# Kernel optimization log

Measured on AMD Instinct MI355X. Metric: run time of the kernel, lower is better.

Reference implementation:

```python
import jax, jax.numpy as jnp
import numpy as np

B, T, TEMP, H, M = 2048, 168, 128, 1024, 48


def lstm_cell(x, h, c, Wih, Whh, bih, bhh):
    # PyTorch gate order: i, f, g, o
    gates = x @ Wih.T + h @ Whh.T + bih + bhh  # [B, 4H]
    i, f, g, o = jnp.split(gates, 4, axis=-1)
    i = jax.nn.sigmoid(i)
    f = jax.nn.sigmoid(f)
    g = jnp.tanh(g)
    o = jax.nn.sigmoid(o)
    c_new = f * c + i * g
    h_new = o * jnp.tanh(c_new)
    return h_new, c_new


def setup_inputs() -> dict:
    key = jax.random.key(0)
    ks = jax.random.split(key, 12)
    s_e = 1.0 / np.sqrt(H)
    u = lambda k, shape: jax.random.uniform(k, shape, jnp.float32, -s_e, s_e)
    return {
        "temp_seq": jax.random.normal(ks[0], (B, T, TEMP), jnp.float32),
        "avg_speeds": jax.random.normal(ks[1], (B, M), jnp.float32),
        "enc_Wih": u(ks[2], (4 * H, TEMP)),
        "enc_Whh": u(ks[3], (4 * H, H)),
        "enc_bih": u(ks[4], (4 * H,)),
        "enc_bhh": u(ks[5], (4 * H,)),
        "dec_Wih": u(ks[6], (4 * H, TEMP + 1)),
        "dec_Whh": u(ks[7], (4 * H, H)),
        "dec_bih": u(ks[8], (4 * H,)),
        "dec_bhh": u(ks[9], (4 * H,)),
        "fc_W": u(ks[10], (TEMP, H)),
        "fc_b": u(ks[11], (TEMP,)),
    }


def reference(temp_seq, avg_speeds, enc_Wih, enc_Whh, enc_bih, enc_bhh,
              dec_Wih, dec_Whh, dec_bih, dec_bhh, fc_W, fc_b):
    b = temp_seq.shape[0]
    h0 = jnp.zeros((b, H), temp_seq.dtype)
    c0 = jnp.zeros((b, H), temp_seq.dtype)

    # Encoder: LSTM over time, keep only final (h, c)
    def enc_step(carry, x_t):
        h, c = carry
        h, c = lstm_cell(x_t, h, c, enc_Wih, enc_Whh, enc_bih, enc_bhh)
        return (h, c), None

    (h_n, c_n), _ = jax.lax.scan(enc_step, (h0, c0), jnp.swapaxes(temp_seq, 0, 1))

    input_temp0 = temp_seq[:, -1, :]  # [B, TEMP]

    def dec_step(carry, speed_t):
        h, c, x_temp = carry
        x = jnp.concatenate([x_temp, speed_t[:, None]], axis=-1)  # [B, TEMP+1]
        h, c = lstm_cell(x, h, c, dec_Wih, dec_Whh, dec_bih, dec_bhh)
        pred = h @ fc_W.T + fc_b  # [B, TEMP]
        return (h, c, pred), pred

    _, preds = jax.lax.scan(dec_step, (h_n, c_n, input_temp0),
                            jnp.swapaxes(avg_speeds, 0, 1))
    return jnp.swapaxes(preds, 0, 1)  # [B, M, TEMP]
```

## Files before the change

### kernel.cpp

```cpp
#include <hip/hip_runtime.h>
#include <stdint.h>

#define B_SZ   2048
#define T_ENC  168
#define TEMPD  128
#define HID    1024
#define M_DEC  48

typedef _Float16 f16;
typedef _Float16 half8 __attribute__((ext_vector_type(8)));
typedef float    f32x4 __attribute__((ext_vector_type(4)));

__device__ __forceinline__ float sigf(float x)   { return 1.0f / (1.0f + __expf(-x)); }
__device__ __forceinline__ float tanhf_(float x) { return 2.0f / (1.0f + __expf(-2.0f * x)) - 1.0f; }

__device__ __forceinline__ void gld16(const void* g, void* l) {
    __builtin_amdgcn_global_load_lds(
        (const __attribute__((address_space(1))) void*)g,
        (__attribute__((address_space(3))) void*)l, 16, 0, 0);
}

#define WAITV6() asm volatile("s_waitcnt vmcnt(6)" ::: "memory")
#define WAITV0() asm volatile("s_waitcnt vmcnt(0)" ::: "memory")
#define SBAR()   do { __builtin_amdgcn_sched_barrier(0); \
                      __builtin_amdgcn_s_barrier();      \
                      __builtin_amdgcn_sched_barrier(0); } while (0)

__global__ void prep_xseq(const float* __restrict__ temp_seq, f16* __restrict__ xseq)
{
    size_t i4 = ((size_t)blockIdx.x * blockDim.x + threadIdx.x) * 4;
    size_t b  = i4 / (T_ENC * TEMPD);
    size_t r  = i4 - b * (T_ENC * TEMPD);
    size_t t  = r >> 7;
    size_t d  = r & 127;
    float4 v = *(const float4*)(temp_seq + i4);
    f16* o = xseq + ((t * B_SZ) + b) * TEMPD + d;
    o[0] = (f16)v.x; o[1] = (f16)v.y; o[2] = (f16)v.z; o[3] = (f16)v.w;
}

__global__ void prep_misc(
    const float* __restrict__ encWih, const float* __restrict__ encWhh,
    const float* __restrict__ decWih, const float* __restrict__ decWhh,
    const float* __restrict__ encbih, const float* __restrict__ encbhh,
    const float* __restrict__ decbih, const float* __restrict__ decbhh,
    const float* __restrict__ fcW,
    f16* __restrict__ Wenc, f16* __restrict__ Wdec0, f16* __restrict__ fcWh,
    float* __restrict__ enc_b, float* __restrict__ dec_b, float* __restrict__ wlast)
{
    const int NW = 4 * HID * (TEMPD + HID);
    for (int idx = blockIdx.x * blockDim.x + threadIdx.x; idx < NW;
         idx += gridDim.x * blockDim.x) {
        int j = idx / (TEMPD + HID);
        int k = idx - j * (TEMPD + HID);
        Wenc[idx]  = (f16)(k < TEMPD ? encWih[j * TEMPD + k]
                                     : encWhh[(size_t)j * HID + (k - TEMPD)]);
        Wdec0[idx] = (f16)(k < TEMPD ? decWih[j * (TEMPD + 1) + k]
                                     : decWhh[(size_t)j * HID + (k - TEMPD)]);
        if (idx < TEMPD * HID) fcWh[idx] = (f16)fcW[idx];
        if (idx < 4 * HID) {
            enc_b[idx] = encbih[idx] + encbhh[idx];
            dec_b[idx] = decbih[idx] + decbhh[idx];
            wlast[idx] = decWih[idx * (TEMPD + 1) + TEMPD];
        }
    }
}

__global__ __launch_bounds__(256)
void prep_fold(
    const float* __restrict__ decWih, const float* __restrict__ decWhh,
    const float* __restrict__ decbih, const float* __restrict__ decbhh,
    const float* __restrict__ fcW,    const float* __restrict__ fcb,
    f16* __restrict__ WdecF, float* __restrict__ biasF)
{
    __shared__ float wih[16][TEMPD];
    __shared__ float fcbL[TEMPD];
    const int tid = threadIdx.x;
    const int j0  = blockIdx.x * 16;
    for (int i = tid; i < 16 * TEMPD; i += 256) {
        int r = i >> 7, p = i & 127;
        wih[r][p] = decWih[(size_t)(j0 + r) * (TEMPD + 1) + p];
    }
    if (tid < TEMPD) fcbL[tid] = fcb[tid];
    __syncthreads();
    for (int kk = 0; kk < 4; ++kk) {
        int k = kk * 256 + tid;
        float acc[16];
        #pragma unroll
        for (int r = 0; r < 16; ++r) acc[r] = decWhh[(size_t)(j0 + r) * HID + k];
        for (int p = 0; p < TEMPD; ++p) {
            float w = fcW[(size_t)p * HID + k];
            #pragma unroll
            for (int r = 0; r < 16; ++r) acc[r] += wih[r][p] * w;
        }
        #pragma unroll
        for (int r = 0; r < 16; ++r) WdecF[(size_t)(j0 + r) * HID + k] = (f16)acc[r];
    }
    if (tid < 16) {
        float b = decbih[j0 + tid] + decbhh[j0 + tid];
        for (int p = 0; p < TEMPD; ++p) b += wih[tid][p] * fcbL[p];
        biasF[j0 + tid] = b;
    }
}

template <int FULLK, int DEC>
__global__ __launch_bounds__(512, 2)
void lstm_step(
    const f16* __restrict__ xsrc,
    const f16* __restrict__ h_in, f16* __restrict__ h_out, float* __restrict__ c,
    const f16* __restrict__ W,
    const float* __restrict__ bias,
    const float* __restrict__ wlast, const float* __restrict__ speeds, int m_step)
{
    constexpr int NKC = FULLK ? 18 : 16;
    constexpr int WS  = FULLK ? (HID + TEMPD) : HID;

    __shared__ half8 ldsA[3][1024];
    __shared__ half8 ldsW[3][2048];

    const int tid  = threadIdx.x;
    const int id   = blockIdx.x;
    const int swzb = (id & 7) * 32 + (id >> 3);
    const int bm   = swzb & 15;
    const int bn   = swzb >> 4;
    const int lane = tid & 63;
    const int wid  = tid >> 6;
    const int wr   = wid >> 2;
    const int wc   = wid & 3;

    f32x4 acc[4][4];
    #pragma unroll
    for (int g = 0; g < 4; ++g)
        #pragma unroll
        for (int mr = 0; mr < 4; ++mr)
            acc[g][mr] = (f32x4){0.f, 0.f, 0.f, 0.f};

    auto stageA = [&](int b, int kc) {
        if (FULLK && kc < 2) {
            #pragma unroll
            for (int it = 0; it < 2; ++it) {
                int p = wid * 128 + it * 64 + lane;
                int row = p >> 3, s = p & 7;
                gld16(xsrc + (size_t)(bm * 128 + row) * TEMPD + kc * 64 + ((s ^ (row & 7)) << 3),
                      &ldsA[b][wid * 128 + it * 64]);
            }
        } else {
            const int k0 = kc * 64 - (FULLK ? TEMPD : 0);
            #pragma unroll
            for (int it = 0; it < 2; ++it) {
                int p = wid * 128 + it * 64 + lane;
                int row = p >> 3, s = p & 7;
                gld16(h_in + (size_t)(bm * 128 + row) * HID + k0 + ((s ^ (row & 7)) << 3),
                      &ldsA[b][wid * 128 + it * 64]);
            }
        }
    };
    auto stageW = [&](int b, int kc) {
        const int k0 = kc * 64;
        #pragma unroll
        for (int it = 0; it < 4; ++it) {
            int p = wid * 256 + it * 64 + lane;
            int r = p >> 3, s = p & 7;
            int g = r >> 6, j = r & 63;
            gld16(W + (size_t)(g * HID + bn * 64 + j) * WS + k0 + ((s ^ (r & 7)) << 3),
                  &ldsW[b][wid * 256 + it * 64]);
        }
    };

    stageA(0, 0); stageW(0, 0);
    stageA(1, 1); stageW(1, 1);

    int cur = 0;
    for (int kc = 0; kc < NKC; ++kc) {
        if (kc == NKC - 1) { WAITV0(); } else { WAITV6(); }
        SBAR();
        if (kc + 2 < NKC) {
            int nb = cur + 2; if (nb >= 3) nb -= 3;
            stageA(nb, kc + 2);
            stageW(nb, kc + 2);
        }
        #pragma unroll
        for (int s = 0; s < 2; ++s) {
            const int ks = s * 4 + (lane >> 4);
            half8 af[4];
            #pragma unroll
            for (int mr = 0; mr < 4; ++mr) {
                int row = wr * 64 + mr * 16 + (lane & 15);
                af[mr] = ldsA[cur][row * 8 + (ks ^ (row & 7))];
            }
            half8 bf[4];
            #pragma unroll
            for (int g = 0; g < 4; ++g) {
                int r = g * 64 + wc * 16 + (lane & 15);
                bf[g] = ldsW[cur][r * 8 + (ks ^ (r & 7))];
            }
            __builtin_amdgcn_s_setprio(1);
            #pragma unroll
            for (int g = 0; g < 4; ++g)
                #pragma unroll
                for (int mr = 0; mr < 4; ++mr)
                    acc[g][mr] = __builtin_amdgcn_mfma_f32_16x16x32_f16(af[mr], bf[g], acc[g][mr], 0, 0, 0);
            __builtin_amdgcn_s_setprio(0);
        }
        cur = (cur == 2) ? 0 : cur + 1;
    }

    const int col_g = bn * 64 + wc * 16 + (lane & 15);
    const float bi  = bias[col_g];
    const float bf_ = bias[HID + col_g];
    const float bg  = bias[2 * HID + col_g];
    const float bo  = bias[3 * HID + col_g];
    float wli = 0.f, wlf = 0.f, wlg = 0.f, wlo = 0.f;
    if (DEC) {
        wli = wlast[col_g];
        wlf = wlast[HID + col_g];
        wlg = wlast[2 * HID + col_g];
        wlo = wlast[3 * HID + col_g];
    }
    #pragma unroll
    for (int mr = 0; mr < 4; ++mr) {
        #pragma unroll
        for (int q = 0; q < 4; ++q) {
            int row_g = bm * 128 + wr * 64 + mr * 16 + (lane >> 4) * 4 + q;
            float pi = acc[0][mr][q] + bi;
            float pf = acc[1][mr][q] + bf_;
            float pg = acc[2][mr][q] + bg;
            float po = acc[3][mr][q] + bo;
            if (DEC) {
                float sp = speeds[(size_t)row_g * M_DEC + m_step];
                pi += sp * wli; pf += sp * wlf; pg += sp * wlg; po += sp * wlo;
            }
            float ii = sigf(pi), ff = sigf(pf), gg = tanhf_(pg), oo = sigf(po);
            size_t idx = (size_t)row_g * HID + col_g;
            float cn = ff * c[idx] + ii * gg;
            c[idx] = cn;
            h_out[idx] = (f16)(oo * tanhf_(cn));
        }
    }
}

__global__ __launch_bounds__(256, 2)
void fc_batch(const f16* __restrict__ hist, const f16* __restrict__ fcWh,
              const float* __restrict__ fcb, float* __restrict__ out, int mbase)
{
    __shared__ half8 ldsA[32 * 8];
    __shared__ half8 ldsW[128 * 8];
    const int tid  = threadIdx.x;
    const int lane = tid & 63;
    const int wid  = tid >> 6;
    const int wr   = wid >> 1;
    const int wc   = wid & 1;
    const int bm   = blockIdx.x;
    const int slot = bm >> 6;
    const int b0   = (bm & 63) * 32;
    const f16* hrow = hist + (size_t)slot * (B_SZ * HID) + (size_t)b0 * HID;
    const int  mm   = mbase + slot;

    f32x4 acc[4];
    #pragma unroll
    for (int nr = 0; nr < 4; ++nr) acc[nr] = (f32x4){0.f, 0.f, 0.f, 0.f};

    for (int kc = 0; kc < HID / 64; ++kc) {
        const int k0 = kc * 64;
        {
            int row = tid >> 3, s = tid & 7;
            gld16(hrow + (size_t)row * HID + k0 + ((s ^ (row & 7)) << 3), &ldsA[wid * 64]);
        }
        #pragma unroll
        for (int it = 0; it < 4; ++it) {
            int p = wid * 256 + it * 64 + lane;
            int row = p >> 3, s = p & 7;
            gld16(fcWh + (size_t)row * HID + k0 + ((s ^ (row & 7)) << 3), &ldsW[wid * 256 + it * 64]);
        }
        __syncthreads();
        #pragma unroll
        for (int s2 = 0; s2 < 2; ++s2) {
            int arow = wr * 16 + (lane & 15);
            int slotk = s2 * 4 + (lane >> 4);
            half8 a = ldsA[arow * 8 + (slotk ^ (arow & 7))];
            #pragma unroll
            for (int nr = 0; nr < 4; ++nr) {
                int brow = wc * 64 + nr * 16 + (lane & 15);
                half8 bfr = ldsW[brow * 8 + (slotk ^ (brow & 7))];
                acc[nr] = __builtin_amdgcn_mfma_f32_16x16x32_f16(a, bfr, acc[nr], 0, 0, 0);
            }
        }
        __syncthreads();
    }
    #pragma unroll
    for (int nr = 0; nr < 4; ++nr)
        #pragma unroll
        for (int q = 0; q < 4; ++q) {
            int rloc = wr * 16 + (lane >> 4) * 4 + q;
            int col  = wc * 64 + nr * 16 + (lane & 15);
            out[(size_t)(b0 + rloc) * (M_DEC * TEMPD) + (size_t)mm * TEMPD + col] = acc[nr][q] + fcb[col];
        }
}

extern "C" void kernel_launch(void* const* d_in, const int* in_sizes, int n_in,
                              void* d_out, int out_size, void* d_ws, size_t ws_size,
                              hipStream_t stream)
{
    (void)in_sizes; (void)n_in; (void)out_size; (void)ws_size;
    const float* temp_seq   = (const float*)d_in[0];
    const float* avg_speeds = (const float*)d_in[1];
    const float* enc_Wih    = (const float*)d_in[2];
    const float* enc_Whh    = (const float*)d_in[3];
    const float* enc_bih    = (const float*)d_in[4];
    const float* enc_bhh    = (const float*)d_in[5];
    const float* dec_Wih    = (const float*)d_in[6];
    const float* dec_Whh    = (const float*)d_in[7];
    const float* dec_bih    = (const float*)d_in[8];
    const float* dec_bhh    = (const float*)d_in[9];
    const float* fc_W       = (const float*)d_in[10];
    const float* fc_b       = (const float*)d_in[11];
    float* out = (float*)d_out;

    char* ws = (char*)d_ws;
    size_t off = 0;
    auto alloc = [&](size_t bytes) -> void* {
        void* p = ws + off;
        off += (bytes + 255) & ~(size_t)255;
        return p;
    };
    const size_t SLOT = (size_t)B_SZ * HID;
    f16*   Wenc   = (f16*)alloc((size_t)4 * HID * (TEMPD + HID) * 2);
    f16*   Wdec0  = (f16*)alloc((size_t)4 * HID * (TEMPD + HID) * 2);
    f16*   WdecF  = (f16*)alloc((size_t)4 * HID * HID * 2);
    f16*   fcWh   = (f16*)alloc((size_t)TEMPD * HID * 2);
    float* enc_b  = (float*)alloc((size_t)4 * HID * 4);
    float* dec_b  = (float*)alloc((size_t)4 * HID * 4);
    float* biasF  = (float*)alloc((size_t)4 * HID * 4);
    float* wlast  = (float*)alloc((size_t)4 * HID * 4);
    f16*   hA     = (f16*)alloc(SLOT * 2);
    f16*   hB     = (f16*)alloc(SLOT * 2);
    float* cbuf   = (float*)alloc(SLOT * 4);
    f16*   xseq   = (f16*)alloc((size_t)T_ENC * B_SZ * TEMPD * 2);
    f16*   hist   = (f16*)alloc(16 * SLOT * 2);

    hipMemsetAsync(hA,   0, SLOT * 2, stream);
    hipMemsetAsync(cbuf, 0, SLOT * 4, stream);

    prep_xseq<<<(B_SZ * T_ENC * TEMPD / 4 + 255) / 256, 256, 0, stream>>>(temp_seq, xseq);
    prep_misc<<<8192, 256, 0, stream>>>(
        enc_Wih, enc_Whh, dec_Wih, dec_Whh,
        enc_bih, enc_bhh, dec_bih, dec_bhh, fc_W,
        Wenc, Wdec0, fcWh, enc_b, dec_b, wlast);
    prep_fold<<<256, 256, 0, stream>>>(
        dec_Wih, dec_Whh, dec_bih, dec_bhh, fc_W, fc_b, WdecF, biasF);

    f16* hbuf[2] = {hA, hB};
    for (int t = 0; t < T_ENC; ++t) {
        lstm_step<1, 0><<<256, 512, 0, stream>>>(
            xseq + (size_t)t * (B_SZ * TEMPD),
            hbuf[t & 1], hbuf[(t + 1) & 1], cbuf,
            Wenc, enc_b, nullptr, nullptr, 0);
    }
    for (int m = 0; m < M_DEC; ++m) {
        const f16* hin = (m == 0) ? hA : hist + ((size_t)((m - 1) & 15)) * SLOT;
        f16* hout = hist + ((size_t)(m & 15)) * SLOT;
        if (m == 0) {
            lstm_step<1, 1><<<256, 512, 0, stream>>>(
                xseq + (size_t)(T_ENC - 1) * (B_SZ * TEMPD),
                hin, hout, cbuf, Wdec0, dec_b, wlast, avg_speeds, 0);
        } else {
            lstm_step<0, 1><<<256, 512, 0, stream>>>(
                nullptr, hin, hout, cbuf, WdecF, biasF, wlast, avg_speeds, m);
        }
        if ((m & 15) == 15) {
            fc_batch<<<1024, 256, 0, stream>>>(hist, fcWh, fc_b, out, m - 15);
        }
    }
}
```

Baseline: 6.821 ms.

## Interleave split weight staging with fragment reads and MFMA, prefetch cell state

The LSTM gate GEMM main loop is restructured. Each K-chunk now reads LDS fragments and issues MFMAs in two halves, and the next chunk's weight staging is split across those halves, with explicit lgkmcnt waits and barriers between them. The c state and decoder speed values are loaded into registers before the loop, so the epilogue no longer waits on those global loads. The goal is better overlap of global-to-LDS traffic with MFMA work. In exchange it adds four barriers per chunk instead of one, and 32 more live registers under a two-blocks-per-CU launch bound.

```diff
diff --git a/kernel.cpp b/kernel.cpp
--- a/kernel.cpp
+++ b/kernel.cpp
@@ -25,6 +25,9 @@
 #define SBAR()   do { __builtin_amdgcn_sched_barrier(0); \
                       __builtin_amdgcn_s_barrier();      \
                       __builtin_amdgcn_sched_barrier(0); } while (0)
+#define LGKM0()  do { asm volatile("s_waitcnt lgkmcnt(0)" ::: "memory"); \
+                      __builtin_amdgcn_sched_barrier(0); } while (0)
+#define MEMFENCE() asm volatile("" ::: "memory")
 
 __global__ void prep_xseq(const float* __restrict__ temp_seq, f16* __restrict__ xseq)
 {
@@ -154,10 +157,11 @@
             }
         }
     };
-    auto stageW = [&](int b, int kc) {
+    auto stageWhalf = [&](int b, int kc, int half) {
         const int k0 = kc * 64;
         #pragma unroll
-        for (int it = 0; it < 4; ++it) {
+        for (int it2 = 0; it2 < 2; ++it2) {
+            int it = half * 2 + it2;
             int p = wid * 256 + it * 64 + lane;
             int r = p >> 3, s = p & 7;
             int g = r >> 6, j = r & 63;
@@ -166,43 +170,32 @@
         }
     };
 
-    stageA(0, 0); stageW(0, 0);
-    stageA(1, 1); stageW(1, 1);
-
-    int cur = 0;
-    for (int kc = 0; kc < NKC; ++kc) {
-        if (kc == NKC - 1) { WAITV0(); } else { WAITV6(); }
-        SBAR();
-        if (kc + 2 < NKC) {
-            int nb = cur + 2; if (nb >= 3) nb -= 3;
-            stageA(nb, kc + 2);
-            stageW(nb, kc + 2);
-        }
-        #pragma unroll
-        for (int s = 0; s < 2; ++s) {
-            const int ks = s * 4 + (lane >> 4);
-            half8 af[4];
+    half8 af[4], bf[4];
+    auto rdfrags = [&](int cb, int s) {
+        const int ks = s * 4 + (lane >> 4);
+        #pragma unroll
+        for (int mr = 0; mr < 4; ++mr) {
+            int row = wr * 64 + mr * 16 + (lane & 15);
+            af[mr] = ldsA[cb][row * 8 + (ks ^ (row & 7))];
+        }
+        #pragma unroll
+        for (int g = 0; g < 4; ++g) {
+            int r = g * 64 + wc * 16 + (lane & 15);
+            bf[g] = ldsW[cb][r * 8 + (ks ^ (r & 7))];
+        }
+    };
+    auto mfma16 = [&]() {
+        __builtin_amdgcn_s_setprio(1);
+        #pragma unroll
+        for (int g = 0; g < 4; ++g)
             #pragma unroll
-            for (int mr = 0; mr < 4; ++mr) {
-                int row = wr * 64 + mr * 16 + (lane & 15);
-                af[mr] = ldsA[cur][row * 8 + (ks ^ (row & 7))];
-            }
-            half8 bf[4];
-            #pragma unroll
-            for (int g = 0; g < 4; ++g) {
-                int r = g * 64 + wc * 16 + (lane & 15);
-                bf[g] = ldsW[cur][r * 8 + (ks ^ (r & 7))];
-            }
-            __builtin_amdgcn_s_setprio(1);
-            #pragma unroll
-            for (int g = 0; g < 4; ++g)
-                #pragma unroll
-                for (int mr = 0; mr < 4; ++mr)
-                    acc[g][mr] = __builtin_amdgcn_mfma_f32_16x16x32_f16(af[mr], bf[g], acc[g][mr], 0, 0, 0);
-            __builtin_amdgcn_s_setprio(0);
-        }
-        cur = (cur == 2) ? 0 : cur + 1;
-    }
+            for (int mr = 0; mr < 4; ++mr)
+                acc[g][mr] = __builtin_amdgcn_mfma_f32_16x16x32_f16(af[mr], bf[g], acc[g][mr], 0, 0, 0);
+        __builtin_amdgcn_s_setprio(0);
+    };
+
+    stageA(0, 0); stageWhalf(0, 0, 0); stageWhalf(0, 0, 1);
+    MEMFENCE();
 
     const int col_g = bn * 64 + wc * 16 + (lane & 15);
     const float bi  = bias[col_g];
@@ -210,12 +203,53 @@
     const float bg  = bias[2 * HID + col_g];
     const float bo  = bias[3 * HID + col_g];
     float wli = 0.f, wlf = 0.f, wlg = 0.f, wlo = 0.f;
+    float sp_r[4];
     if (DEC) {
         wli = wlast[col_g];
         wlf = wlast[HID + col_g];
         wlg = wlast[2 * HID + col_g];
         wlo = wlast[3 * HID + col_g];
-    }
+        #pragma unroll
+        for (int mr = 0; mr < 4; ++mr) {
+            int row_g = bm * 128 + wr * 64 + mr * 16 + (lane >> 4) * 4;
+            sp_r[mr] = 0.f;
+            (void)row_g;
+        }
+    }
+    float creg[4][4];
+    float spq[4][4];
+    #pragma unroll
+    for (int mr = 0; mr < 4; ++mr)
+        #pragma unroll
+        for (int q = 0; q < 4; ++q) {
+            int row_g = bm * 128 + wr * 64 + mr * 16 + (lane >> 4) * 4 + q;
+            creg[mr][q] = c[(size_t)row_g * HID + col_g];
+            if (DEC) spq[mr][q] = speeds[(size_t)row_g * M_DEC + m_step];
+        }
+
+    stageA(1, 1); stageWhalf(1, 1, 0); stageWhalf(1, 1, 1);
+    WAITV6();
+    SBAR();
+
+    int cur = 0;
+    for (int kc = 0; kc < NKC; ++kc) {
+        int nb = cur + 2; if (nb >= 3) nb -= 3;
+        rdfrags(cur, 0);
+        if (kc + 2 < NKC) { stageA(nb, kc + 2); stageWhalf(nb, kc + 2, 0); }
+        SBAR();
+        LGKM0();
+        mfma16();
+        SBAR();
+        rdfrags(cur, 1);
+        if (kc + 2 < NKC) { stageWhalf(nb, kc + 2, 1); WAITV6(); }
+        else              { WAITV0(); }
+        SBAR();
+        LGKM0();
+        mfma16();
+        SBAR();
+        cur = (cur == 2) ? 0 : cur + 1;
+    }
+
     #pragma unroll
     for (int mr = 0; mr < 4; ++mr) {
         #pragma unroll
@@ -226,12 +260,12 @@
             float pg = acc[2][mr][q] + bg;
             float po = acc[3][mr][q] + bo;
             if (DEC) {
-                float sp = speeds[(size_t)row_g * M_DEC + m_step];
+                float sp = spq[mr][q];
                 pi += sp * wli; pf += sp * wlf; pg += sp * wlg; po += sp * wlo;
             }
             float ii = sigf(pi), ff = sigf(pf), gg = tanhf_(pg), oo = sigf(po);
             size_t idx = (size_t)row_g * HID + col_g;
-            float cn = ff * c[idx] + ii * gg;
+            float cn = ff * creg[mr][q] + ii * gg;
             c[idx] = cn;
             h_out[idx] = (f16)(oo * tanhf_(cn));
         }
```

New measurement: 6.273 ms. 8.0% less time.

## Load pre-tiled LSTM weights directly into registers and drop LDS weight staging

Applied to the files above, without the earlier changes.

Adds a prep kernel that rearranges the gate weight matrices into MFMA-fragment order, so each wave can read its B operands straight from global memory into registers instead of staging them through LDS. The step kernel moves to 256-thread blocks covering 32 hidden columns, with 512 blocks per step, and switches from a three-stage pipeline with explicit vmcnt waits to two LDS buffers for the activations only, synchronised with __syncthreads. This cuts LDS traffic and footprint, which may allow more resident blocks. In exchange, each weight element is fetched by more blocks and register pressure goes up because two fragment sets are held in flight.

```diff
diff --git a/kernel.cpp b/kernel.cpp
--- a/kernel.cpp
+++ b/kernel.cpp
@@ -19,12 +19,6 @@
         (const __attribute__((address_space(1))) void*)g,
         (__attribute__((address_space(3))) void*)l, 16, 0, 0);
 }
-
-#define WAITV6() asm volatile("s_waitcnt vmcnt(6)" ::: "memory")
-#define WAITV0() asm volatile("s_waitcnt vmcnt(0)" ::: "memory")
-#define SBAR()   do { __builtin_amdgcn_sched_barrier(0); \
-                      __builtin_amdgcn_s_barrier();      \
-                      __builtin_amdgcn_sched_barrier(0); } while (0)
 
 __global__ void prep_xseq(const float* __restrict__ temp_seq, f16* __restrict__ xseq)
 {
@@ -102,30 +96,48 @@
     }
 }
 
+__global__ void prep_tileW(const f16* __restrict__ Wsrc, f16* __restrict__ Wt,
+                           int NKC, int WS)
+{
+    int idx = blockIdx.x * blockDim.x + threadIdx.x;
+    int total = 32 * NKC * 16 * 64;
+    if (idx >= total) return;
+    int lane = idx & 63;
+    int f    = idx >> 6;
+    int wc   = f & 1;
+    int g    = (f >> 1) & 3;
+    int s    = (f >> 3) & 1;
+    int kc   = (f >> 4) % NKC;
+    int bn   = (f >> 4) / NKC;
+    int row  = g * HID + bn * 32 + wc * 16 + (lane & 15);
+    int k0   = kc * 64 + s * 32 + (lane >> 4) * 8;
+    *(half8*)(Wt + (size_t)idx * 8) = *(const half8*)(Wsrc + (size_t)row * WS + k0);
+}
+
 template <int FULLK, int DEC>
-__global__ __launch_bounds__(512, 2)
+__global__ __launch_bounds__(256, 2)
 void lstm_step(
     const f16* __restrict__ xsrc,
     const f16* __restrict__ h_in, f16* __restrict__ h_out, float* __restrict__ c,
-    const f16* __restrict__ W,
+    const f16* __restrict__ Wt,
     const float* __restrict__ bias,
     const float* __restrict__ wlast, const float* __restrict__ speeds, int m_step)
 {
     constexpr int NKC = FULLK ? 18 : 16;
-    constexpr int WS  = FULLK ? (HID + TEMPD) : HID;
-
-    __shared__ half8 ldsA[3][1024];
-    __shared__ half8 ldsW[3][2048];
+
+    __shared__ half8 ldsA[2][1024];
 
     const int tid  = threadIdx.x;
-    const int id   = blockIdx.x;
-    const int swzb = (id & 7) * 32 + (id >> 3);
-    const int bm   = swzb & 15;
-    const int bn   = swzb >> 4;
     const int lane = tid & 63;
     const int wid  = tid >> 6;
-    const int wr   = wid >> 2;
-    const int wc   = wid & 3;
+    const int wr   = wid >> 1;
+    const int wc   = wid & 1;
+    const int id   = blockIdx.x;
+    const int swzb = (id & 7) * 64 + (id >> 3);
+    const int bn   = swzb >> 4;
+    const int bm   = swzb & 15;
+
+    const half8* wtb = (const half8*)Wt + ((size_t)bn * NKC * 16) * 64 + wc * 64 + lane;
 
     f32x4 acc[4][4];
     #pragma unroll
@@ -137,47 +149,29 @@
     auto stageA = [&](int b, int kc) {
         if (FULLK && kc < 2) {
             #pragma unroll
-            for (int it = 0; it < 2; ++it) {
-                int p = wid * 128 + it * 64 + lane;
+            for (int it = 0; it < 4; ++it) {
+                int p = wid * 256 + it * 64 + lane;
                 int row = p >> 3, s = p & 7;
                 gld16(xsrc + (size_t)(bm * 128 + row) * TEMPD + kc * 64 + ((s ^ (row & 7)) << 3),
-                      &ldsA[b][wid * 128 + it * 64]);
+                      &ldsA[b][wid * 256 + it * 64]);
             }
         } else {
             const int k0 = kc * 64 - (FULLK ? TEMPD : 0);
             #pragma unroll
-            for (int it = 0; it < 2; ++it) {
-                int p = wid * 128 + it * 64 + lane;
+            for (int it = 0; it < 4; ++it) {
+                int p = wid * 256 + it * 64 + lane;
                 int row = p >> 3, s = p & 7;
                 gld16(h_in + (size_t)(bm * 128 + row) * HID + k0 + ((s ^ (row & 7)) << 3),
-                      &ldsA[b][wid * 128 + it * 64]);
+                      &ldsA[b][wid * 256 + it * 64]);
             }
         }
     };
-    auto stageW = [&](int b, int kc) {
-        const int k0 = kc * 64;
-        #pragma unroll
-        for (int it = 0; it < 4; ++it) {
-            int p = wid * 256 + it * 64 + lane;
-            int r = p >> 3, s = p & 7;
-            int g = r >> 6, j = r & 63;
-            gld16(W + (size_t)(g * HID + bn * 64 + j) * WS + k0 + ((s ^ (r & 7)) << 3),
-                  &ldsW[b][wid * 256 + it * 64]);
-        }
+    auto loadW = [&](half8 (&wf)[8], int kc) {
+        const half8* p = wtb + (size_t)kc * (16 * 64);
+        #pragma unroll
+        for (int f = 0; f < 8; ++f) wf[f] = p[f * 128];
     };
-
-    stageA(0, 0); stageW(0, 0);
-    stageA(1, 1); stageW(1, 1);
-
-    int cur = 0;
-    for (int kc = 0; kc < NKC; ++kc) {
-        if (kc == NKC - 1) { WAITV0(); } else { WAITV6(); }
-        SBAR();
-        if (kc + 2 < NKC) {
-            int nb = cur + 2; if (nb >= 3) nb -= 3;
-            stageA(nb, kc + 2);
-            stageW(nb, kc + 2);
-        }
+    auto compute = [&](int b, const half8 (&wf)[8]) {
         #pragma unroll
         for (int s = 0; s < 2; ++s) {
             const int ks = s * 4 + (lane >> 4);
@@ -185,26 +179,32 @@
             #pragma unroll
             for (int mr = 0; mr < 4; ++mr) {
                 int row = wr * 64 + mr * 16 + (lane & 15);
-                af[mr] = ldsA[cur][row * 8 + (ks ^ (row & 7))];
-            }
-            half8 bf[4];
-            #pragma unroll
-            for (int g = 0; g < 4; ++g) {
-                int r = g * 64 + wc * 16 + (lane & 15);
-                bf[g] = ldsW[cur][r * 8 + (ks ^ (r & 7))];
+                af[mr] = ldsA[b][row * 8 + (ks ^ (row & 7))];
             }
             __builtin_amdgcn_s_setprio(1);
             #pragma unroll
             for (int g = 0; g < 4; ++g)
                 #pragma unroll
                 for (int mr = 0; mr < 4; ++mr)
-                    acc[g][mr] = __builtin_amdgcn_mfma_f32_16x16x32_f16(af[mr], bf[g], acc[g][mr], 0, 0, 0);
+                    acc[g][mr] = __builtin_amdgcn_mfma_f32_16x16x32_f16(af[mr], wf[s * 4 + g], acc[g][mr], 0, 0, 0);
             __builtin_amdgcn_s_setprio(0);
         }
-        cur = (cur == 2) ? 0 : cur + 1;
-    }
-
-    const int col_g = bn * 64 + wc * 16 + (lane & 15);
+    };
+
+    half8 wfA[8], wfB[8];
+    stageA(0, 0); loadW(wfA, 0);
+    __syncthreads();
+
+    for (int kc = 0; kc < NKC; kc += 2) {
+        stageA(1, kc + 1); loadW(wfB, kc + 1);
+        compute(0, wfA);
+        __syncthreads();
+        if (kc + 2 < NKC) { stageA(0, kc + 2); loadW(wfA, kc + 2); }
+        compute(1, wfB);
+        __syncthreads();
+    }
+
+    const int col_g = bn * 32 + wc * 16 + (lane & 15);
     const float bi  = bias[col_g];
     const float bf_ = bias[HID + col_g];
     const float bg  = bias[2 * HID + col_g];
@@ -326,6 +326,9 @@
     f16*   Wenc   = (f16*)alloc((size_t)4 * HID * (TEMPD + HID) * 2);
     f16*   Wdec0  = (f16*)alloc((size_t)4 * HID * (TEMPD + HID) * 2);
     f16*   WdecF  = (f16*)alloc((size_t)4 * HID * HID * 2);
+    f16*   WencT  = (f16*)alloc((size_t)32 * 18 * 16 * 64 * 8 * 2);
+    f16*   Wdec0T = (f16*)alloc((size_t)32 * 18 * 16 * 64 * 8 * 2);
+    f16*   WdecFT = (f16*)alloc((size_t)32 * 16 * 16 * 64 * 8 * 2);
     f16*   fcWh   = (f16*)alloc((size_t)TEMPD * HID * 2);
     float* enc_b  = (float*)alloc((size_t)4 * HID * 4);
     float* dec_b  = (float*)alloc((size_t)4 * HID * 4);
@@ -347,24 +350,27 @@
         Wenc, Wdec0, fcWh, enc_b, dec_b, wlast);
     prep_fold<<<256, 256, 0, stream>>>(
         dec_Wih, dec_Whh, dec_bih, dec_bhh, fc_W, fc_b, WdecF, biasF);
+    prep_tileW<<<(32 * 18 * 16 * 64 + 255) / 256, 256, 0, stream>>>(Wenc,  WencT,  18, TEMPD + HID);
+    prep_tileW<<<(32 * 18 * 16 * 64 + 255) / 256, 256, 0, stream>>>(Wdec0, Wdec0T, 18, TEMPD + HID);
+    prep_tileW<<<(32 * 16 * 16 * 64 + 255) / 256, 256, 0, stream>>>(WdecF, WdecFT, 16, HID);
 
     f16* hbuf[2] = {hA, hB};
     for (int t = 0; t < T_ENC; ++t) {
-        lstm_step<1, 0><<<256, 512, 0, stream>>>(
+        lstm_step<1, 0><<<512, 256, 0, stream>>>(
             xseq + (size_t)t * (B_SZ * TEMPD),
             hbuf[t & 1], hbuf[(t + 1) & 1], cbuf,
-            Wenc, enc_b, nullptr, nullptr, 0);
+            WencT, enc_b, nullptr, nullptr, 0);
     }
     for (int m = 0; m < M_DEC; ++m) {
         const f16* hin = (m == 0) ? hA : hist + ((size_t)((m - 1) & 15)) * SLOT;
         f16* hout = hist + ((size_t)(m & 15)) * SLOT;
         if (m == 0) {
-            lstm_step<1, 1><<<256, 512, 0, stream>>>(
+            lstm_step<1, 1><<<512, 256, 0, stream>>>(
                 xseq + (size_t)(T_ENC - 1) * (B_SZ * TEMPD),
-                hin, hout, cbuf, Wdec0, dec_b, wlast, avg_speeds, 0);
+                hin, hout, cbuf, Wdec0T, dec_b, wlast, avg_speeds, 0);
         } else {
-            lstm_step<0, 1><<<256, 512, 0, stream>>>(
-                nullptr, hin, hout, cbuf, WdecF, biasF, wlast, avg_speeds, m);
+            lstm_step<0, 1><<<512, 256, 0, stream>>>(
+                nullptr, hin, hout, cbuf, WdecFT, biasF, wlast, avg_speeds, m);
         }
         if ((m & 15) == 15) {
             fc_batch<<<1024, 256, 0, stream>>>(hist, fcWh, fc_b, out, m - 15);
```

Measured after the change: 6.319 ms. 7.4% less time.
